# Kernel optimization log

Hardware: AMD Instinct MI355X
Metric: run time of the kernel (lower is better)

The kernel has to match this reference:

```python
import jax, jax.numpy as jnp
import numpy as np


def setup_inputs() -> dict:
    key = jax.random.key(0)
    k1, k2 = jax.random.split(key)
    B, C, H, W, T = 64, 128, 8, 8, 100
    outputs = jax.random.normal(k1, (B, C, H, W, T), dtype=jnp.float32)
    target = jax.random.uniform(k2, (B, C, H, W, T), dtype=jnp.float32)
    return {"outputs": outputs, "target": target, "n_steps": T, "tau_s": 2}


def _psp(x, tau_s):
    # x: [B, C, H, W, T]; fixed-coefficient leaky integrator over last axis.
    # syn_t = syn_{t-1} * (1 - 1/tau_s) + x_t ; out_t = syn_t / tau_s
    decay = 1.0 - 1.0 / tau_s
    xt = jnp.moveaxis(x, -1, 0)  # [T, B, C, H, W]

    def step(syn, x_t):
        syn = syn * decay + x_t
        return syn, syn / tau_s

    syn0 = jnp.zeros(x.shape[:-1], dtype=x.dtype)
    _, syns = jax.lax.scan(step, syn0, xt)
    return jnp.moveaxis(syns, 0, -1)  # [B, C, H, W, T]


def reference(outputs, target, n_steps, tau_s):
    # n_steps is implied by the trailing axis; kept for signature fidelity.
    target_psp = _psp(target, float(tau_s))
    delta = outputs - target_psp
    return 0.5 * jnp.sum(delta * delta)
```

## Files before the change

kernel.cpp:

```cpp
#include <hip/hip_runtime.h>


constexpr int T   = 100;
constexpr int PIX = 16;
constexpr int TF  = PIX * T;
constexpr int NCH = (TF * 4) / 1024;

typedef const __attribute__((address_space(1))) void* gas_t;
typedef __attribute__((address_space(3))) void*       las_t;
typedef float f4 __attribute__((ext_vector_type(4)));

__global__ __launch_bounds__(64) void spike_loss_kernel(
    const float* __restrict__ tgt,
    const float* __restrict__ outs,
    const int*   __restrict__ tau_p,
    float*       __restrict__ out,
    int n_tiles, int tiles_per_block)
{
    __shared__ __align__(16) float lds_t[2][TF];
    __shared__ __align__(16) float lds_o[2][TF];

    const float tau     = (float)tau_p[0];
    const float inv_tau = 1.0f / tau;
    const float decay   = 1.0f - inv_tau;
    float d28 = 1.0f;
    #pragma unroll
    for (int i = 0; i < 28; ++i) d28 *= decay;
    const float d56 = d28 * d28;

    const int tid = threadIdx.x;

    const int first = blockIdx.x * tiles_per_block;
    int cnt = n_tiles - first;
    if (cnt < 0) cnt = 0;
    if (cnt > tiles_per_block) cnt = tiles_per_block;
    if (cnt <= 0) return;

    float acc = 0.0f;

    auto stage = [&](int tile, int buf) {
        const float* gt = tgt  + (size_t)tile * TF;
        const float* go = outs + (size_t)tile * TF;
        #pragma unroll
        for (int c = 0; c < NCH; ++c) {
            __builtin_amdgcn_global_load_lds((gas_t)(gt + c * 256 + tid * 4),
                (las_t)&lds_t[buf][c * 256], 16, 0, 0);
            __builtin_amdgcn_global_load_lds((gas_t)(go + c * 256 + tid * 4),
                (las_t)&lds_o[buf][c * 256], 16, 0, 0);
        }
        __builtin_amdgcn_global_load_lds((gas_t)(gt + NCH * 256 + tid),
            (las_t)&lds_t[buf][NCH * 256], 4, 0, 0);
        __builtin_amdgcn_global_load_lds((gas_t)(go + NCH * 256 + tid),
            (las_t)&lds_o[buf][NCH * 256], 4, 0, 0);
    };

    auto consume = [&](int buf) {
        const int p  = tid >> 2;
        const int q  = tid & 3;
        const int fb = p * T + q * 28;
        const f4* tb = (const f4*)&lds_t[buf][fb];
        const f4* ob = (const f4*)&lds_o[buf][fb];
        const int segn = (q == 3) ? 16 : 28;

        float s[28];
        float syn = 0.0f;
        #pragma unroll
        for (int j = 0; j < 7; ++j) {
            if (j * 4 < segn) {
                const f4 v = tb[j];
                #pragma unroll
                for (int c = 0; c < 4; ++c) {
                    syn = fmaf(syn, decay, v[c]);
                    s[j * 4 + c] = syn;
                }
            }
        }
        const float f1 = __shfl_up(syn, 1, 64);
        const float f2 = __shfl_up(syn, 2, 64);
        const float f3 = __shfl_up(syn, 3, 64);
        float carry = (q >= 1) ? f1 : 0.0f;
        if (q >= 2) carry = fmaf(f2, d28, carry);
        if (q >= 3) carry = fmaf(f3, d56, carry);

        float cp = carry;
        #pragma unroll
        for (int j = 0; j < 7; ++j) {
            if (j * 4 < segn) {
                const f4 ov = ob[j];
                #pragma unroll
                for (int c = 0; c < 4; ++c) {
                    cp *= decay;
                    const float st = s[j * 4 + c] + cp;
                    const float d  = fmaf(st, -inv_tau, ov[c]);
                    acc = fmaf(d, d, acc);
                }
            }
        }
    };

    stage(first, 0);

    for (int k = 0; k < cnt; ++k) {
        const int buf = k & 1;
        if (k + 1 < cnt) {
            stage(first + k + 1, buf ^ 1);
            asm volatile("s_waitcnt vmcnt(14)" ::: "memory");
        } else {
            asm volatile("s_waitcnt vmcnt(0)" ::: "memory");
        }
        consume(buf);
        asm volatile("s_waitcnt lgkmcnt(0)" ::: "memory");
    }

    #pragma unroll
    for (int off = 32; off > 0; off >>= 1)
        acc += __shfl_down(acc, off, 64);
    if (tid == 0)
        atomicAdd(out, 0.5f * acc);
}

extern "C" void kernel_launch(void* const* d_in, const int* in_sizes, int n_in,
                              void* d_out, int out_size, void* d_ws, size_t ws_size,
                              hipStream_t stream) {
    const float* outs = (const float*)d_in[0];
    const float* tgt  = (const float*)d_in[1];
    const int* tau_p  = (const int*)d_in[3];
    float* out        = (float*)d_out;

    const int n_pixels = in_sizes[0] / T;
    const int n_tiles  = n_pixels / PIX;

    const int block = 64;
    const int grid  = 1536;
    const int tiles_per_block = (n_tiles + grid - 1) / grid;

    hipMemsetAsync(out, 0, sizeof(float), stream);

    spike_loss_kernel<<<grid, block, 0, stream>>>(
        tgt, outs, tau_p, out, n_tiles, tiles_per_block);
}
```

Before: 419.2 us.

## Register-prefetch tiles, stage only target in LDS, double grid size

Replaces the direct global-to-LDS async loads with coalesced vector loads into registers, double-buffered two tiles ahead. Only the target goes through LDS: it is written there, scanned in place with the PSP values written back, then read coalesced and compared against the outputs still held in registers. This halves the LDS footprint and doubles the grid to raise occupancy. The cost is much higher register pressure and extra LDS write and read passes with more waitcnt barriers.

```diff
diff --git a/kernel.cpp b/kernel.cpp
--- a/kernel.cpp
+++ b/kernel.cpp
@@ -4,21 +4,17 @@
 constexpr int T   = 100;
 constexpr int PIX = 16;
 constexpr int TF  = PIX * T;
-constexpr int NCH = (TF * 4) / 1024;
 
-typedef const __attribute__((address_space(1))) void* gas_t;
-typedef __attribute__((address_space(3))) void*       las_t;
 typedef float f4 __attribute__((ext_vector_type(4)));
 
-__global__ __launch_bounds__(64) void spike_loss_kernel(
+__global__ __launch_bounds__(64, 3) void spike_loss_kernel(
     const float* __restrict__ tgt,
     const float* __restrict__ outs,
     const int*   __restrict__ tau_p,
     float*       __restrict__ out,
     int n_tiles, int tiles_per_block)
 {
-    __shared__ __align__(16) float lds_t[2][TF];
-    __shared__ __align__(16) float lds_o[2][TF];
+    __shared__ __align__(16) float lds[2][TF];
 
     const float tau     = (float)tau_p[0];
     const float inv_tau = 1.0f / tau;
@@ -38,35 +34,39 @@
 
     float acc = 0.0f;
 
-    auto stage = [&](int tile, int buf) {
-        const float* gt = tgt  + (size_t)tile * TF;
-        const float* go = outs + (size_t)tile * TF;
+    auto issue = [&](int tile, f4 (&tr)[7], f4 (&orr)[7]) {
+        const f4* gt = (const f4*)(tgt  + (size_t)tile * TF);
+        const f4* go = (const f4*)(outs + (size_t)tile * TF);
         #pragma unroll
-        for (int c = 0; c < NCH; ++c) {
-            __builtin_amdgcn_global_load_lds((gas_t)(gt + c * 256 + tid * 4),
-                (las_t)&lds_t[buf][c * 256], 16, 0, 0);
-            __builtin_amdgcn_global_load_lds((gas_t)(go + c * 256 + tid * 4),
-                (las_t)&lds_o[buf][c * 256], 16, 0, 0);
+        for (int j = 0; j < 6; ++j) {
+            tr[j]  = gt[tid + 64 * j];
+            orr[j] = go[tid + 64 * j];
         }
-        __builtin_amdgcn_global_load_lds((gas_t)(gt + NCH * 256 + tid),
-            (las_t)&lds_t[buf][NCH * 256], 4, 0, 0);
-        __builtin_amdgcn_global_load_lds((gas_t)(go + NCH * 256 + tid),
-            (las_t)&lds_o[buf][NCH * 256], 4, 0, 0);
+        if (tid < 16) {
+            tr[6]  = gt[384 + tid];
+            orr[6] = go[384 + tid];
+        }
     };
 
-    auto consume = [&](int buf) {
+    auto write_lds = [&](int buf, f4 (&tr)[7]) {
+        f4* d = (f4*)lds[buf];
+        #pragma unroll
+        for (int j = 0; j < 6; ++j) d[tid + 64 * j] = tr[j];
+        if (tid < 16) d[384 + tid] = tr[6];
+    };
+
+    auto scan = [&](int buf) {
         const int p  = tid >> 2;
         const int q  = tid & 3;
         const int fb = p * T + q * 28;
-        const f4* tb = (const f4*)&lds_t[buf][fb];
-        const f4* ob = (const f4*)&lds_o[buf][fb];
-        const int segn = (q == 3) ? 16 : 28;
+        f4* tb = (f4*)&lds[buf][fb];
+        const int nf4 = (q == 3) ? 4 : 7;
 
         float s[28];
         float syn = 0.0f;
         #pragma unroll
         for (int j = 0; j < 7; ++j) {
-            if (j * 4 < segn) {
+            if (j < nf4) {
                 const f4 v = tb[j];
                 #pragma unroll
                 for (int c = 0; c < 4; ++c) {
@@ -85,31 +85,65 @@
         float cp = carry;
         #pragma unroll
         for (int j = 0; j < 7; ++j) {
-            if (j * 4 < segn) {
-                const f4 ov = ob[j];
+            if (j < nf4) {
+                f4 w;
                 #pragma unroll
                 for (int c = 0; c < 4; ++c) {
                     cp *= decay;
-                    const float st = s[j * 4 + c] + cp;
-                    const float d  = fmaf(st, -inv_tau, ov[c]);
-                    acc = fmaf(d, d, acc);
+                    w[c] = s[j * 4 + c] + cp;
                 }
+                tb[j] = w;
             }
         }
     };
 
-    stage(first, 0);
+    auto pass2 = [&](int buf, f4 (&orr)[7]) {
+        const f4* p4 = (const f4*)lds[buf];
+        #pragma unroll
+        for (int j = 0; j < 6; ++j) {
+            const f4 sy = p4[tid + 64 * j];
+            #pragma unroll
+            for (int c = 0; c < 4; ++c) {
+                const float d = fmaf(sy[c], -inv_tau, orr[j][c]);
+                acc = fmaf(d, d, acc);
+            }
+        }
+        if (tid < 16) {
+            const f4 sy = p4[384 + tid];
+            #pragma unroll
+            for (int c = 0; c < 4; ++c) {
+                const float d = fmaf(sy[c], -inv_tau, orr[6][c]);
+                acc = fmaf(d, d, acc);
+            }
+        }
+    };
 
-    for (int k = 0; k < cnt; ++k) {
-        const int buf = k & 1;
-        if (k + 1 < cnt) {
-            stage(first + k + 1, buf ^ 1);
-            asm volatile("s_waitcnt vmcnt(14)" ::: "memory");
-        } else {
-            asm volatile("s_waitcnt vmcnt(0)" ::: "memory");
-        }
-        consume(buf);
+    f4 tA[7], oA[7], tB[7], oB[7];
+
+    issue(first, tA, oA);
+    if (cnt > 1) issue(first + 1, tB, oB);
+    write_lds(0, tA);
+    asm volatile("s_waitcnt lgkmcnt(0)" ::: "memory");
+
+    int k = 0;
+    while (true) {
+        scan(0);
         asm volatile("s_waitcnt lgkmcnt(0)" ::: "memory");
+        pass2(0, oA);
+        if (k + 1 >= cnt) break;
+        write_lds(1, tB);
+        if (k + 2 < cnt) issue(first + k + 2, tA, oA);
+        asm volatile("s_waitcnt lgkmcnt(0)" ::: "memory");
+        ++k;
+
+        scan(1);
+        asm volatile("s_waitcnt lgkmcnt(0)" ::: "memory");
+        pass2(1, oB);
+        if (k + 1 >= cnt) break;
+        write_lds(0, tA);
+        if (k + 2 < cnt) issue(first + k + 2, tB, oB);
+        asm volatile("s_waitcnt lgkmcnt(0)" ::: "memory");
+        ++k;
     }
 
     #pragma unroll
@@ -131,7 +165,7 @@
     const int n_tiles  = n_pixels / PIX;
 
     const int block = 64;
-    const int grid  = 1536;
+    const int grid  = 3072;
     const int tiles_per_block = (n_tiles + grid - 1) / grid;
 
     hipMemsetAsync(out, 0, sizeof(float), stream);
```

After: 419.5 us. Within noise of the previous version (+0.1%).
